# Kernel tuning notes

Hardware: AMD Instinct MI355X
Metric: run time of the kernel (lower is better)

## Reference

```python
import jax, jax.numpy as jnp
import numpy as np

N_MFS = 2
N_FEATURES = 12
OUTPUT_DIM = 8
BATCH = 4096
N_RULES = N_MFS ** N_FEATURES  # 4096


def _rule_indices(n_features, n_mfs):
    r = np.arange(n_mfs ** n_features)
    # mixed-radix digits: indices[rule, feat] = (rule // n_mfs**feat) % n_mfs
    return np.stack([(r // (n_mfs ** f)) % n_mfs for f in range(n_features)], axis=1).astype(np.int32)


def setup_inputs() -> dict:
    key = jax.random.key(0)
    ks = jax.random.split(key, 6)
    x = jax.random.normal(ks[0], (BATCH, N_FEATURES), dtype=jnp.float32)
    center_base = jax.random.uniform(ks[1], (N_FEATURES, 1), minval=-1.0, maxval=0.0, dtype=jnp.float32)
    center_delta_raw = jax.random.normal(ks[2], (N_FEATURES, N_MFS - 1), dtype=jnp.float32) * 0.5
    width_raw = jax.random.normal(ks[3], (N_FEATURES, N_MFS), dtype=jnp.float32) * 0.5
    fan = N_RULES * N_FEATURES + OUTPUT_DIM
    limit = float(np.sqrt(6.0 / fan))
    consequent_p = jax.random.uniform(ks[4], (N_RULES, N_FEATURES, OUTPUT_DIM), minval=-limit, maxval=limit, dtype=jnp.float32)
    consequent_r = jnp.zeros((N_RULES, OUTPUT_DIM), dtype=jnp.float32)
    rule_mf_indices = jnp.asarray(_rule_indices(N_FEATURES, N_MFS))
    return {"x": x, "center_base": center_base, "center_delta_raw": center_delta_raw,
            "width_raw": width_raw, "consequent_p": consequent_p, "consequent_r": consequent_r,
            "rule_mf_indices": rule_mf_indices}


def reference(x, center_base, center_delta_raw, width_raw, consequent_p, consequent_r, rule_mf_indices):
    # ordered centers: base + cumsum(softplus(delta) + 1e-3)
    gaps = jax.nn.softplus(center_delta_raw) + 1e-3          # (F, M-1)
    offsets = jnp.cumsum(gaps, axis=1)
    centers = jnp.concatenate([center_base, center_base + offsets], axis=1)  # (F, M)
    widths = jax.nn.softplus(width_raw) + 1e-3                # (F, M)

    # Gaussian memberships: (B, F, M)
    d = x[:, :, None] - centers[None, :, :]
    memberships = jnp.exp(-jnp.square(d) / (2.0 * jnp.square(widths)[None, :, :]))

    # rule firing: product over features of gathered memberships (loop over small fixed F)
    firing = jnp.ones((x.shape[0], rule_mf_indices.shape[0]), dtype=x.dtype)  # (B, R)
    for f in range(memberships.shape[1]):
        firing = firing * memberships[:, f, :][:, rule_mf_indices[:, f]]
    firing_norm = firing / (jnp.sum(firing, axis=1, keepdims=True) + 1e-8)

    # per-rule linear consequents: (B, R, O)
    rule_outputs = jnp.einsum('bf,rfo->bro', x, consequent_p) + consequent_r[None, :, :]
    # weighted reduce over rules: (B, O)
    output = jnp.einsum('br,bro->bo', firing_norm, rule_outputs)
    return output
```

## Files before the change

### kernel.cpp

```cpp
#include <hip/hip_runtime.h>
#include <math.h>

#define NF 12
#define NB 4096
#define NR 4096
#define NO 8

typedef float f32x4v __attribute__((ext_vector_type(4)));
typedef short bf16x8 __attribute__((ext_vector_type(8)));
typedef unsigned int uint32x4 __attribute__((ext_vector_type(4)));

#define PT2_BYTES (128 * 8 * 512 * 2)
#define PARAMS_OFF PT2_BYTES
#define WS_NEED (PT2_BYTES + 2048)
#define PT_ELEMS (112 * 4096)

__device__ __forceinline__ float softplus_f(float v) {
    return fmaxf(v, 0.0f) + log1pf(__expf(-fabsf(v)));
}
__device__ __forceinline__ unsigned short f2bf(float f) {
    unsigned u = __float_as_uint(f);
    u += 0x7FFFu + ((u >> 16) & 1u);
    return (unsigned short)(u >> 16);
}
__device__ __forceinline__ unsigned cvt_pk_bf16(float a, float b) {
    unsigned r;
    asm("v_cvt_pk_bf16_f32 %0, %1, %2" : "=v"(r) : "v"(a), "v"(b));
    return r;
}

__device__ __forceinline__ void build_split(f32x4v va, f32x4v vb,
                                            bf16x8& ah, bf16x8& al) {
    unsigned h0 = cvt_pk_bf16(va[0], va[1]), h1 = cvt_pk_bf16(va[2], va[3]);
    unsigned h2 = cvt_pk_bf16(vb[0], vb[1]), h3 = cvt_pk_bf16(vb[2], vb[3]);
    f32x4v hia = { __uint_as_float(h0 << 16), __uint_as_float(h0 & 0xFFFF0000u),
                   __uint_as_float(h1 << 16), __uint_as_float(h1 & 0xFFFF0000u) };
    f32x4v hib = { __uint_as_float(h2 << 16), __uint_as_float(h2 & 0xFFFF0000u),
                   __uint_as_float(h3 << 16), __uint_as_float(h3 & 0xFFFF0000u) };
    f32x4v ea = va - hia;
    f32x4v eb = vb - hib;
    unsigned q0 = cvt_pk_bf16(ea[0], ea[1]), q1 = cvt_pk_bf16(ea[2], ea[3]);
    unsigned q2 = cvt_pk_bf16(eb[0], eb[1]), q3 = cvt_pk_bf16(eb[2], eb[3]);
    union { uint32x4 u; bf16x8 v; } A, B;
    A.u = (uint32x4){h0, h1, h2, h3};
    B.u = (uint32x4){q0, q1, q2, q3};
    ah = A.v; al = B.v;
}

__global__ __launch_bounds__(512) void anfis_prep2(
    const float* __restrict__ cp, const float* __restrict__ cr,
    const float* __restrict__ center_base, const float* __restrict__ cdr,
    const float* __restrict__ wr,
    unsigned short* __restrict__ PT2, float* __restrict__ params,
    float* __restrict__ out_zero)
{
    __shared__ float s_cp[32 * 97];
    __shared__ float s_cr[32 * 8];
    const int kt = blockIdx.x;
    const int tid = threadIdx.x;

    if (kt < 64) out_zero[(size_t)kt * 512 + tid] = 0.0f;

    {
        const float4* cp4 = (const float4*)(cp + (size_t)kt * 32 * 96);
        for (int i = tid; i < 768; i += 512) {
            float4 v = cp4[i];
            int r = i / 24, c4 = i - r * 24;
            float* d = &s_cp[r * 97 + c4 * 4];
            d[0] = v.x; d[1] = v.y; d[2] = v.z; d[3] = v.w;
        }
        if (tid < 64) {
            float4 v = ((const float4*)(cr + (size_t)kt * 32 * 8))[tid];
            float* d = &s_cr[tid * 4];
            d[0] = v.x; d[1] = v.y; d[2] = v.z; d[3] = v.w;
        }
    }
    __syncthreads();

    const int g = tid >> 7, col = (tid >> 3) & 15, e = tid & 7;
    const int rr = g * 8 + e;
    #pragma unroll
    for (int j = 0; j < 8; ++j) {
        int n = j * 16 + col;
        float v = 0.f;
        if (n < 96) v = s_cp[rr * 97 + n];
        else if (n < 104) v = s_cr[rr * 8 + (n - 96)];
        PT2[(size_t)(kt * 8 + j) * 512 + tid] = f2bf(v);
    }

    if (kt == 0 && tid < NF) {
        float c0 = center_base[tid];
        float gap = softplus_f(cdr[tid]) + 1e-3f;
        float w0 = softplus_f(wr[tid * 2 + 0]) + 1e-3f;
        float w1 = softplus_f(wr[tid * 2 + 1]) + 1e-3f;
        params[tid * 4 + 0] = c0;
        params[tid * 4 + 1] = c0 + gap;
        params[tid * 4 + 2] = -0.5f / (w0 * w0);
        params[tid * 4 + 3] = -0.5f / (w1 * w1);
    }
}

__global__ __launch_bounds__(512, 4) void anfis_main7(
    const float* __restrict__ x,
    const unsigned short* __restrict__ PT2,
    const float* __restrict__ params,
    float* __restrict__ out)
{
    __shared__ float s_params[48];
    __shared__ float s_mf[64 * 24];
    __shared__ float s_prod[64 * 8];
    __shared__ float s_rcp[64];
    __shared__ float s_x[64 * 12];
    __shared__ float s_low[64 * 36];
    __shared__ float s_highT[16 * 64];
    __shared__ __align__(16) unsigned char s_B[2 * 16384];

    const int tid = threadIdx.x;
    const int bid = blockIdx.x;
    const int ks = bid & 7;
    const int mt = bid >> 3;
    const int b0 = mt * 64;
    const int kt0 = ks * 16;

    const int w = tid >> 6, l = tid & 63;

    const unsigned char* ptBase = (const unsigned char*)PT2;
    #define STAGE(c, buf) do {                                                        \
        if (w != 7) {                                                                 \
            const unsigned char* gb = ptBase + ((size_t)(kt0 + 2 * (c)) << 13);       \
            unsigned char* lb = &s_B[(buf) * 16384];                                  \
            __builtin_amdgcn_global_load_lds(                                         \
                (const __attribute__((address_space(1))) void*)(gb + w * 1024 + l * 16),  \
                (__attribute__((address_space(3))) void*)(lb + w * 1024), 16, 0, 0);  \
            __builtin_amdgcn_global_load_lds(                                         \
                (const __attribute__((address_space(1))) void*)(gb + (8 + w) * 1024 + l * 16), \
                (__attribute__((address_space(3))) void*)(lb + (8 + w) * 1024), 16, 0, 0);\
        }                                                                             \
    } while (0)

    STAGE(0, 0);
    STAGE(1, 1);

    if (tid < 192) {
        float4 v = ((const float4*)(x + (size_t)b0 * NF))[tid];
        float* d = &s_x[tid * 4];
        d[0] = v.x; d[1] = v.y; d[2] = v.z; d[3] = v.w;
    }
    if (tid >= 500) {
        int f = tid - 500;
        ((float4*)s_params)[f] = ((const float4*)params)[f];
    }
    __syncthreads();

    if (tid < 384) {
        int row = tid / 6, fp = tid - row * 6;
        float pr = 1.f;
        #pragma unroll
        for (int h = 0; h < 2; ++h) {
            int f = fp + h * 6;
            float xv = s_x[row * 12 + f];
            float4 pm = *(const float4*)&s_params[f * 4];
            float d0 = xv - pm.x, d1 = xv - pm.y;
            float m0 = __expf(d0 * d0 * pm.z);
            float m1 = __expf(d1 * d1 * pm.w);
            s_mf[row * 24 + f * 2 + 0] = m0;
            s_mf[row * 24 + f * 2 + 1] = m1;
            pr *= (m0 + m1);
        }
        s_prod[row * 8 + fp] = pr;
    }
    __syncthreads();
    if (tid < 64) {
        float S = 1.f;
        #pragma unroll
        for (int i = 0; i < 6; ++i) S *= s_prod[tid * 8 + i];
        s_rcp[tid] = 1.0f / (S + 1e-8f);
    }
    __syncthreads();

    {
        int row = tid >> 3, w8 = tid & 7;
        const float* mr = &s_mf[row * 24];
        #pragma unroll
        for (int i = 0; i < 4; ++i) {
            int ee = w8 * 4 + i;
            float p = 1.f;
            #pragma unroll
            for (int f = 0; f < 5; ++f) p *= mr[f * 2 + ((ee >> f) & 1)];
            s_low[row * 36 + ee] = p;
        }
        float rc = s_rcp[row];
        #pragma unroll
        for (int i = 0; i < 2; ++i) {
            int t = w8 * 2 + i;
            int ktg = kt0 + t;
            float p = rc;
            #pragma unroll
            for (int ff = 0; ff < 7; ++ff) p *= mr[(5 + ff) * 2 + ((ktg >> ff) & 1)];
            s_highT[t * 64 + row] = p;
        }
    }
    __syncthreads();

    const int rp = w >> 2, cq = w & 3;
    const int col = l & 15, g = l >> 4;
    const int nj = (cq < 3) ? 2 : 1;
    const int jb = cq * 2;

    bf16x8 ah[2], al[2];
    #pragma unroll
    for (int i = 0; i < 2; ++i) {
        int rowA = (rp * 2 + i) * 16 + col;
        f32x4v lo0 = *(const f32x4v*)&s_low[rowA * 36 + g * 8];
        f32x4v lo1 = *(const f32x4v*)&s_low[rowA * 36 + g * 8 + 4];
        build_split(lo0, lo1, ah[i], al[i]);
    }

    f32x4v acc[2][2];
    #pragma unroll
    for (int i = 0; i < 2; ++i)
        #pragma unroll
        for (int jj = 0; jj < 2; ++jj) acc[i][jj] = (f32x4v){0.f, 0.f, 0.f, 0.f};
    const f32x4v z4 = (f32x4v){0.f, 0.f, 0.f, 0.f};

    const int hoff0 = (rp * 2 + 0) * 16 + g * 4;
    const int hoff1 = (rp * 2 + 1) * 16 + g * 4;

    #pragma unroll 1
    for (int c = 0; c < 8; ++c) {
        const int cur = c & 1;
        if (c >= 1 && c + 1 < 8) STAGE(c + 1, cur ^ 1);
        #pragma unroll
        for (int kt2 = 0; kt2 < 2; ++kt2) {
            const int t = c * 2 + kt2;
            const unsigned char* base = &s_B[cur * 16384 + kt2 * 8192 + l * 16];
            bf16x8 fr0 = *(const bf16x8*)(base + jb * 1024);
            f32x4v hv0 = *(const f32x4v*)&s_highT[t * 64 + hoff0];
            f32x4v hv1 = *(const f32x4v*)&s_highT[t * 64 + hoff1];
            f32x4v q00, q10;
            q00 = __builtin_amdgcn_mfma_f32_16x16x32_bf16(ah[0], fr0, z4, 0, 0, 0);
            q00 = __builtin_amdgcn_mfma_f32_16x16x32_bf16(al[0], fr0, q00, 0, 0, 0);
            q10 = __builtin_amdgcn_mfma_f32_16x16x32_bf16(ah[1], fr0, z4, 0, 0, 0);
            q10 = __builtin_amdgcn_mfma_f32_16x16x32_bf16(al[1], fr0, q10, 0, 0, 0);
            acc[0][0] += hv0 * q00;
            acc[1][0] += hv1 * q10;
            if (nj == 2) {
                bf16x8 fr1 = *(const bf16x8*)(base + (jb + 1) * 1024);
                f32x4v q01, q11;
                q01 = __builtin_amdgcn_mfma_f32_16x16x32_bf16(ah[0], fr1, z4, 0, 0, 0);
                q01 = __builtin_amdgcn_mfma_f32_16x16x32_bf16(al[0], fr1, q01, 0, 0, 0);
                q11 = __builtin_amdgcn_mfma_f32_16x16x32_bf16(ah[1], fr1, z4, 0, 0, 0);
                q11 = __builtin_amdgcn_mfma_f32_16x16x32_bf16(al[1], fr1, q11, 0, 0, 0);
                acc[0][1] += hv0 * q01;
                acc[1][1] += hv1 * q11;
            }
        }
        __syncthreads();
    }
    #undef STAGE

    float* s_acc = (float*)s_B;
    #pragma unroll
    for (int i = 0; i < 2; ++i) {
        #pragma unroll
        for (int jj = 0; jj < 2; ++jj) {
            if (jj < nj) {
                int j = jb + jj;
                #pragma unroll
                for (int q = 0; q < 4; ++q)
                    s_acc[((rp * 2 + i) * 16 + g * 4 + q) * 116 + j * 16 + col] = acc[i][jj][q];
            }
        }
    }
    __syncthreads();
    {
        const int row = tid >> 3, o = tid & 7;
        const float* ar = &s_acc[row * 116];
        float t = ar[96 + o];
        #pragma unroll
        for (int f = 0; f < NF; ++f) t = fmaf(s_x[row * 12 + f], ar[f * 8 + o], t);
        atomicAdd(&out[(size_t)(b0 + row) * NO + o], t);
    }
}

__global__ __launch_bounds__(256) void anfis_prep(
    const float* __restrict__ cp, const float* __restrict__ cr,
    unsigned short* __restrict__ PT)
{
    const int n = blockIdx.x;
    const int t = threadIdx.x;
    if (n < 96) {
        #pragma unroll
        for (int i = 0; i < 16; ++i) { int r = i * 256 + t; PT[n * 4096 + r] = f2bf(cp[r * 96 + n]); }
    } else if (n < 104) {
        const int o = n - 96;
        #pragma unroll
        for (int i = 0; i < 16; ++i) { int r = i * 256 + t; PT[n * 4096 + r] = f2bf(cr[r * 8 + o]); }
    } else {
        #pragma unroll
        for (int i = 0; i < 16; ++i) PT[n * 4096 + i * 256 + t] = 0;
    }
}

__global__ __launch_bounds__(512) void anfis_mfma(
    const float* __restrict__ x,
    const float* __restrict__ center_base,
    const float* __restrict__ center_delta_raw,
    const float* __restrict__ width_raw,
    const unsigned short* __restrict__ PT,
    float* __restrict__ out)
{
    __shared__ float s_mem[16 * 26];
    __shared__ float s_low[16 * 36];
    __shared__ float s_high[16 * 132];
    __shared__ float s_red[8 * 16 * 113];

    const int tid = threadIdx.x;
    const int b0 = blockIdx.x * 16;

    if (tid < 16) {
        const int b = b0 + tid;
        float S = 1.0f;
        #pragma unroll
        for (int f = 0; f < NF; ++f) {
            float cb  = center_base[f];
            float gap = softplus_f(center_delta_raw[f]) + 1e-3f;
            float c0 = cb, c1 = cb + gap;
            float w0 = softplus_f(width_raw[f * 2 + 0]) + 1e-3f;
            float w1 = softplus_f(width_raw[f * 2 + 1]) + 1e-3f;
            float xv = x[b * NF + f];
            float d0 = xv - c0, d1 = xv - c1;
            float m0 = __expf(-d0 * d0 / (2.0f * w0 * w0));
            float m1 = __expf(-d1 * d1 / (2.0f * w1 * w1));
            s_mem[tid * 26 + f * 2 + 0] = m0;
            s_mem[tid * 26 + f * 2 + 1] = m1;
            S *= (m0 + m1);
        }
        s_mem[tid * 26 + 24] = 1.0f / (S + 1e-8f);
    }
    __syncthreads();
    if (tid < 256) {
        const int row = tid >> 4, w16 = tid & 15;
        const float* mrow = &s_mem[row * 26];
        #pragma unroll
        for (int e = 2 * w16; e <= 2 * w16 + 1; ++e) {
            float p = 1.0f;
            #pragma unroll
            for (int f = 0; f < 5; ++f) p *= mrow[f * 2 + ((e >> f) & 1)];
            s_low[row * 36 + e] = p;
        }
        float rcp = mrow[24];
        #pragma unroll
        for (int i = 0; i < 8; ++i) {
            int e = w16 + 16 * i;
            float p = rcp;
            #pragma unroll
            for (int ff = 0; ff < 7; ++ff) p *= mrow[(5 + ff) * 2 + ((e >> ff) & 1)];
            s_high[row * 132 + e] = p;
        }
    }
    __syncthreads();

    const int w = tid >> 6;
    const int l = tid & 63;
    const int col = l & 15;
    const int g   = l >> 4;

    f32x4v lo0 = *(const f32x4v*)&s_low[col * 36 + g * 8];
    f32x4v lo1 = *(const f32x4v*)&s_low[col * 36 + g * 8 + 4];
    f32x4v hq0 = *(const f32x4v*)&s_high[col * 132 + w * 16 + 0];
    f32x4v hq1 = *(const f32x4v*)&s_high[col * 132 + w * 16 + 4];
    f32x4v hq2 = *(const f32x4v*)&s_high[col * 132 + w * 16 + 8];
    f32x4v hq3 = *(const f32x4v*)&s_high[col * 132 + w * 16 + 12];

    const unsigned short* pB = PT + (size_t)col * 4096 + g * 8 + w * 512;

    f32x4v acc[7];
    #pragma unroll
    for (int j = 0; j < 7; ++j) acc[j] = (f32x4v){0.f, 0.f, 0.f, 0.f};

    bf16x8 bf[2][7];
    #pragma unroll
    for (int j = 0; j < 7; ++j) bf[0][j] = *(const bf16x8*)(pB + j * 65536 + 0 * 32);
    #pragma unroll
    for (int j = 0; j < 7; ++j) bf[1][j] = *(const bf16x8*)(pB + j * 65536 + 1 * 32);

    #pragma unroll
    for (int s = 0; s < 16; ++s) {
        const float hv = (s < 4) ? hq0[s & 3] : (s < 8) ? hq1[s & 3]
                        : (s < 12) ? hq2[s & 3] : hq3[s & 3];
        bf16x8 ah, al;
        #pragma unroll
        for (int e = 0; e < 8; ++e) {
            float v = ((e < 4) ? lo0[e & 3] : lo1[e & 3]) * hv;
            unsigned short h = f2bf(v);
            float vh = __uint_as_float(((unsigned)h) << 16);
            ah[e] = (short)h;
            al[e] = (short)f2bf(v - vh);
        }
        #pragma unroll
        for (int j = 0; j < 7; ++j) {
            acc[j] = __builtin_amdgcn_mfma_f32_16x16x32_bf16(ah, bf[s & 1][j], acc[j], 0, 0, 0);
            acc[j] = __builtin_amdgcn_mfma_f32_16x16x32_bf16(al, bf[s & 1][j], acc[j], 0, 0, 0);
        }
        if (s + 2 < 16) {
            #pragma unroll
            for (int j = 0; j < 7; ++j)
                bf[s & 1][j] = *(const bf16x8*)(pB + j * 65536 + (s + 2) * 32);
        }
    }

    #pragma unroll
    for (int j = 0; j < 7; ++j)
        #pragma unroll
        for (int q = 0; q < 4; ++q)
            s_red[(w * 16 + g * 4 + q) * 113 + j * 16 + col] = acc[j][q];
    __syncthreads();

    if (tid < 128) {
        const int row = tid >> 3, o = tid & 7;
        float xr[NF];
        #pragma unroll
        for (int f = 0; f < NF; ++f) xr[f] = x[(b0 + row) * NF + f];
        float outv = 0.0f;
        #pragma unroll
        for (int ww = 0; ww < 8; ++ww) {
            const float* ar = &s_red[(ww * 16 + row) * 113];
            float t2 = ar[96 + o];
            #pragma unroll
            for (int f = 0; f < NF; ++f) t2 = fmaf(xr[f], ar[f * 8 + o], t2);
            outv += t2;
        }
        out[(b0 + row) * NO + o] = outv;
    }
}

extern "C" void kernel_launch(void* const* d_in, const int* in_sizes, int n_in,
                              void* d_out, int out_size, void* d_ws, size_t ws_size,
                              hipStream_t stream) {
    const float* x   = (const float*)d_in[0];
    const float* cb  = (const float*)d_in[1];
    const float* cdr = (const float*)d_in[2];
    const float* wr  = (const float*)d_in[3];
    const float* cp  = (const float*)d_in[4];
    const float* cr  = (const float*)d_in[5];
    float* out = (float*)d_out;

    if (ws_size >= (size_t)WS_NEED) {
        unsigned short* PT2 = (unsigned short*)d_ws;
        float* params = (float*)((char*)d_ws + PARAMS_OFF);
        anfis_prep2<<<128, 512, 0, stream>>>(cp, cr, cb, cdr, wr, PT2, params, out);
        anfis_main7<<<512, 512, 0, stream>>>(x, PT2, params, out);
    } else if (ws_size >= (size_t)PT_ELEMS * sizeof(unsigned short)) {
        unsigned short* PT = (unsigned short*)d_ws;
        anfis_prep<<<112, 256, 0, stream>>>(cp, cr, PT);
        anfis_mfma<<<NB / 16, 512, 0, stream>>>(x, cb, cdr, wr, PT, out);
    }
}
```

Baseline: 21.27 us.

## Triple-buffer B tiles with explicit vmcnt waits and compute params in-kernel

The rule-table staging loop moves from a double buffer with a full __syncthreads per chunk to a three-slot ring buffer. Each chunk is prefetched two iterations ahead, and consumption is gated by explicit s_waitcnt vmcnt plus a bare s_barrier. The main kernel also computes the softplus membership parameters itself instead of reading them from the prep kernel's workspace. The intent is to overlap global-to-LDS loads with MFMA work and cut sync stalls. In exchange LDS use grows by 16KB per block, which may lower occupancy, and the hand-written vmcnt counting is fragile.

```diff
diff --git a/kernel.cpp b/kernel.cpp
--- a/kernel.cpp
+++ b/kernel.cpp
@@ -100,10 +100,11 @@
     }
 }
 
-__global__ __launch_bounds__(512, 4) void anfis_main7(
+__global__ __launch_bounds__(512, 4) void anfis_main8(
     const float* __restrict__ x,
+    const float* __restrict__ center_base, const float* __restrict__ cdr,
+    const float* __restrict__ wr,
     const unsigned short* __restrict__ PT2,
-    const float* __restrict__ params,
     float* __restrict__ out)
 {
     __shared__ float s_params[48];
@@ -113,7 +114,7 @@
     __shared__ float s_x[64 * 12];
     __shared__ float s_low[64 * 36];
     __shared__ float s_highT[16 * 64];
-    __shared__ __align__(16) unsigned char s_B[2 * 16384];
+    __shared__ __align__(16) unsigned char s_B[3 * 16384];
 
     const int tid = threadIdx.x;
     const int bid = blockIdx.x;
@@ -146,9 +147,16 @@
         float* d = &s_x[tid * 4];
         d[0] = v.x; d[1] = v.y; d[2] = v.z; d[3] = v.w;
     }
-    if (tid >= 500) {
+    if (tid >= 500 && tid < 500 + NF) {
         int f = tid - 500;
-        ((float4*)s_params)[f] = ((const float4*)params)[f];
+        float c0 = center_base[f];
+        float gap = softplus_f(cdr[f]) + 1e-3f;
+        float w0 = softplus_f(wr[f * 2 + 0]) + 1e-3f;
+        float w1 = softplus_f(wr[f * 2 + 1]) + 1e-3f;
+        s_params[f * 4 + 0] = c0;
+        s_params[f * 4 + 1] = c0 + gap;
+        s_params[f * 4 + 2] = -0.5f / (w0 * w0);
+        s_params[f * 4 + 3] = -0.5f / (w1 * w1);
     }
     __syncthreads();
 
@@ -226,14 +234,20 @@
     const int hoff0 = (rp * 2 + 0) * 16 + g * 4;
     const int hoff1 = (rp * 2 + 1) * 16 + g * 4;
 
+    int bc = 0;
     #pragma unroll 1
     for (int c = 0; c < 8; ++c) {
-        const int cur = c & 1;
-        if (c >= 1 && c + 1 < 8) STAGE(c + 1, cur ^ 1);
+        if (c < 7) asm volatile("s_waitcnt vmcnt(2)" ::: "memory");
+        else       asm volatile("s_waitcnt vmcnt(0)" ::: "memory");
+        __builtin_amdgcn_s_barrier();
+        if (c + 2 < 8) {
+            int st = (bc >= 1) ? bc - 1 : 2;
+            STAGE(c + 2, st);
+        }
         #pragma unroll
         for (int kt2 = 0; kt2 < 2; ++kt2) {
             const int t = c * 2 + kt2;
-            const unsigned char* base = &s_B[cur * 16384 + kt2 * 8192 + l * 16];
+            const unsigned char* base = &s_B[bc * 16384 + kt2 * 8192 + l * 16];
             bf16x8 fr0 = *(const bf16x8*)(base + jb * 1024);
             f32x4v hv0 = *(const f32x4v*)&s_highT[t * 64 + hoff0];
             f32x4v hv1 = *(const f32x4v*)&s_highT[t * 64 + hoff1];
@@ -255,9 +269,10 @@
                 acc[1][1] += hv1 * q11;
             }
         }
-        __syncthreads();
+        bc = (bc == 2) ? 0 : bc + 1;
     }
     #undef STAGE
+    __syncthreads();
 
     float* s_acc = (float*)s_B;
     #pragma unroll
@@ -450,7 +465,7 @@
         unsigned short* PT2 = (unsigned short*)d_ws;
         float* params = (float*)((char*)d_ws + PARAMS_OFF);
         anfis_prep2<<<128, 512, 0, stream>>>(cp, cr, cb, cdr, wr, PT2, params, out);
-        anfis_main7<<<512, 512, 0, stream>>>(x, PT2, params, out);
+        anfis_main8<<<512, 512, 0, stream>>>(x, cb, cdr, wr, PT2, out);
     } else if (ws_size >= (size_t)PT_ELEMS * sizeof(unsigned short)) {
         unsigned short* PT = (unsigned short*)d_ws;
         anfis_prep<<<112, 256, 0, stream>>>(cp, cr, PT);
```

After: 21.99 us. +3.4%, slower.

## Replace atomic split-K accumulation with partial buffer and reduction kernel

Applied to the files above, without the earlier changes.

The main kernel now writes per-K-split partial outputs to a workspace buffer instead of atomically adding into the output, and a new small kernel sums the 8 partials. Membership parameters are computed inside the main kernel rather than in the prep kernel. Memberships are kept in registers per thread, which removes two shared-memory passes and barriers. This avoids atomic contention and the need to zero the output, at the cost of an extra kernel launch and extra global traffic for the partials.

```diff
diff --git a/kernel.cpp b/kernel.cpp
--- a/kernel.cpp
+++ b/kernel.cpp
@@ -11,8 +11,9 @@
 typedef unsigned int uint32x4 __attribute__((ext_vector_type(4)));
 
 #define PT2_BYTES (128 * 8 * 512 * 2)
-#define PARAMS_OFF PT2_BYTES
-#define WS_NEED (PT2_BYTES + 2048)
+#define PPART_OFF PT2_BYTES
+#define PPART_BYTES (8 * NB * NO * 4)
+#define WS_NEED (PT2_BYTES + PPART_BYTES)
 #define PT_ELEMS (112 * 4096)
 
 __device__ __forceinline__ float softplus_f(float v) {
@@ -47,19 +48,14 @@
     ah = A.v; al = B.v;
 }
 
-__global__ __launch_bounds__(512) void anfis_prep2(
+__global__ __launch_bounds__(512) void anfis_prep3(
     const float* __restrict__ cp, const float* __restrict__ cr,
-    const float* __restrict__ center_base, const float* __restrict__ cdr,
-    const float* __restrict__ wr,
-    unsigned short* __restrict__ PT2, float* __restrict__ params,
-    float* __restrict__ out_zero)
+    unsigned short* __restrict__ PT2)
 {
     __shared__ float s_cp[32 * 97];
     __shared__ float s_cr[32 * 8];
     const int kt = blockIdx.x;
     const int tid = threadIdx.x;
-
-    if (kt < 64) out_zero[(size_t)kt * 512 + tid] = 0.0f;
 
     {
         const float4* cp4 = (const float4*)(cp + (size_t)kt * 32 * 96);
@@ -87,29 +83,16 @@
         else if (n < 104) v = s_cr[rr * 8 + (n - 96)];
         PT2[(size_t)(kt * 8 + j) * 512 + tid] = f2bf(v);
     }
-
-    if (kt == 0 && tid < NF) {
-        float c0 = center_base[tid];
-        float gap = softplus_f(cdr[tid]) + 1e-3f;
-        float w0 = softplus_f(wr[tid * 2 + 0]) + 1e-3f;
-        float w1 = softplus_f(wr[tid * 2 + 1]) + 1e-3f;
-        params[tid * 4 + 0] = c0;
-        params[tid * 4 + 1] = c0 + gap;
-        params[tid * 4 + 2] = -0.5f / (w0 * w0);
-        params[tid * 4 + 3] = -0.5f / (w1 * w1);
-    }
-}
-
-__global__ __launch_bounds__(512, 4) void anfis_main7(
+}
+
+__global__ __launch_bounds__(512, 4) void anfis_main9(
     const float* __restrict__ x,
+    const float* __restrict__ center_base, const float* __restrict__ cdr,
+    const float* __restrict__ wr,
     const unsigned short* __restrict__ PT2,
-    const float* __restrict__ params,
-    float* __restrict__ out)
+    float* __restrict__ Ppart)
 {
     __shared__ float s_params[48];
-    __shared__ float s_mf[64 * 24];
-    __shared__ float s_prod[64 * 8];
-    __shared__ float s_rcp[64];
     __shared__ float s_x[64 * 12];
     __shared__ float s_low[64 * 36];
     __shared__ float s_highT[16 * 64];
@@ -146,57 +129,52 @@
         float* d = &s_x[tid * 4];
         d[0] = v.x; d[1] = v.y; d[2] = v.z; d[3] = v.w;
     }
-    if (tid >= 500) {
+    if (tid >= 500 && tid < 500 + NF) {
         int f = tid - 500;
-        ((float4*)s_params)[f] = ((const float4*)params)[f];
-    }
-    __syncthreads();
-
-    if (tid < 384) {
-        int row = tid / 6, fp = tid - row * 6;
-        float pr = 1.f;
-        #pragma unroll
-        for (int h = 0; h < 2; ++h) {
-            int f = fp + h * 6;
-            float xv = s_x[row * 12 + f];
+        float c0 = center_base[f];
+        float gap = softplus_f(cdr[f]) + 1e-3f;
+        float w0 = softplus_f(wr[f * 2 + 0]) + 1e-3f;
+        float w1 = softplus_f(wr[f * 2 + 1]) + 1e-3f;
+        s_params[f * 4 + 0] = c0;
+        s_params[f * 4 + 1] = c0 + gap;
+        s_params[f * 4 + 2] = -0.5f / (w0 * w0);
+        s_params[f * 4 + 3] = -0.5f / (w1 * w1);
+    }
+    __syncthreads();
+
+    {
+        const int row = tid >> 3, w8 = tid & 7;
+        const float* xr = &s_x[row * 12];
+        float m0a[NF], m1a[NF];
+        float S = 1.f;
+        #pragma unroll
+        for (int f = 0; f < NF; ++f) {
             float4 pm = *(const float4*)&s_params[f * 4];
+            float xv = xr[f];
             float d0 = xv - pm.x, d1 = xv - pm.y;
-            float m0 = __expf(d0 * d0 * pm.z);
-            float m1 = __expf(d1 * d1 * pm.w);
-            s_mf[row * 24 + f * 2 + 0] = m0;
-            s_mf[row * 24 + f * 2 + 1] = m1;
-            pr *= (m0 + m1);
-        }
-        s_prod[row * 8 + fp] = pr;
-    }
-    __syncthreads();
-    if (tid < 64) {
-        float S = 1.f;
-        #pragma unroll
-        for (int i = 0; i < 6; ++i) S *= s_prod[tid * 8 + i];
-        s_rcp[tid] = 1.0f / (S + 1e-8f);
-    }
-    __syncthreads();
-
-    {
-        int row = tid >> 3, w8 = tid & 7;
-        const float* mr = &s_mf[row * 24];
+            float e0 = __expf(d0 * d0 * pm.z);
+            float e1 = __expf(d1 * d1 * pm.w);
+            m0a[f] = e0; m1a[f] = e1;
+            S *= (e0 + e1);
+        }
+        float rc = 1.0f / (S + 1e-8f);
         #pragma unroll
         for (int i = 0; i < 4; ++i) {
             int ee = w8 * 4 + i;
             float p = 1.f;
             #pragma unroll
-            for (int f = 0; f < 5; ++f) p *= mr[f * 2 + ((ee >> f) & 1)];
+            for (int f = 0; f < 5; ++f)
+                p *= ((ee >> f) & 1) ? m1a[f] : m0a[f];
             s_low[row * 36 + ee] = p;
         }
-        float rc = s_rcp[row];
         #pragma unroll
         for (int i = 0; i < 2; ++i) {
             int t = w8 * 2 + i;
             int ktg = kt0 + t;
             float p = rc;
             #pragma unroll
-            for (int ff = 0; ff < 7; ++ff) p *= mr[(5 + ff) * 2 + ((ktg >> ff) & 1)];
+            for (int ff = 0; ff < 7; ++ff)
+                p *= ((ktg >> ff) & 1) ? m1a[5 + ff] : m0a[5 + ff];
             s_highT[t * 64 + row] = p;
         }
     }
@@ -279,8 +257,22 @@
         float t = ar[96 + o];
         #pragma unroll
         for (int f = 0; f < NF; ++f) t = fmaf(s_x[row * 12 + f], ar[f * 8 + o], t);
-        atomicAdd(&out[(size_t)(b0 + row) * NO + o], t);
-    }
+        Ppart[((size_t)ks * NB + b0 + row) * NO + o] = t;
+    }
+}
+
+__global__ __launch_bounds__(256) void anfis_red2(
+    const float* __restrict__ Ppart, float* __restrict__ out)
+{
+    const int i = blockIdx.x * 256 + threadIdx.x;
+    const float4* p = (const float4*)Ppart;
+    float4 a = p[i];
+    #pragma unroll
+    for (int ksi = 1; ksi < 8; ++ksi) {
+        float4 b = p[(size_t)ksi * (NB * NO / 4) + i];
+        a.x += b.x; a.y += b.y; a.z += b.z; a.w += b.w;
+    }
+    ((float4*)out)[i] = a;
 }
 
 __global__ __launch_bounds__(256) void anfis_prep(
@@ -448,9 +440,10 @@
 
     if (ws_size >= (size_t)WS_NEED) {
         unsigned short* PT2 = (unsigned short*)d_ws;
-        float* params = (float*)((char*)d_ws + PARAMS_OFF);
-        anfis_prep2<<<128, 512, 0, stream>>>(cp, cr, cb, cdr, wr, PT2, params, out);
-        anfis_main7<<<512, 512, 0, stream>>>(x, PT2, params, out);
+        float* Ppart = (float*)((char*)d_ws + PPART_OFF);
+        anfis_prep3<<<128, 512, 0, stream>>>(cp, cr, PT2);
+        anfis_main9<<<512, 512, 0, stream>>>(x, cb, cdr, wr, PT2, Ppart);
+        anfis_red2<<<NB * NO / 4 / 256, 256, 0, stream>>>(Ppart, out);
     } else if (ws_size >= (size_t)PT_ELEMS * sizeof(unsigned short)) {
         unsigned short* PT = (unsigned short*)d_ws;
         anfis_prep<<<112, 256, 0, stream>>>(cp, cr, PT);
```

Measured after the change: 24.49 us. +15.2%, slower.

## Split K across wave halves so each wave covers all 64 rows

Applied to the files above, without the earlier changes.

Each wave previously covered two 16-row A tiles and looped over both k-subtiles per chunk. Now each wave holds all four row tiles and handles only one k-subtile, chosen by wave half. The two halves are then combined through shared memory with an extra barrier-separated accumulate pass. The aim is better reuse of each B fragment across more MFMAs and fewer B fragment reads per MFMA. The cost is more registers for the A fragments and accumulators, plus an added reduction step at the end.

```diff
diff --git a/kernel.cpp b/kernel.cpp
--- a/kernel.cpp
+++ b/kernel.cpp
@@ -100,7 +100,7 @@
     }
 }
 
-__global__ __launch_bounds__(512, 4) void anfis_main7(
+__global__ __launch_bounds__(512, 4) void anfis_main11(
     const float* __restrict__ x,
     const unsigned short* __restrict__ PT2,
     const float* __restrict__ params,
@@ -202,57 +202,56 @@
     }
     __syncthreads();
 
-    const int rp = w >> 2, cq = w & 3;
+    const int h = w >> 2, cq = w & 3;
     const int col = l & 15, g = l >> 4;
     const int nj = (cq < 3) ? 2 : 1;
     const int jb = cq * 2;
 
-    bf16x8 ah[2], al[2];
-    #pragma unroll
-    for (int i = 0; i < 2; ++i) {
-        int rowA = (rp * 2 + i) * 16 + col;
+    bf16x8 ah[4], al[4];
+    #pragma unroll
+    for (int i = 0; i < 4; ++i) {
+        int rowA = i * 16 + col;
         f32x4v lo0 = *(const f32x4v*)&s_low[rowA * 36 + g * 8];
         f32x4v lo1 = *(const f32x4v*)&s_low[rowA * 36 + g * 8 + 4];
         build_split(lo0, lo1, ah[i], al[i]);
     }
 
-    f32x4v acc[2][2];
-    #pragma unroll
-    for (int i = 0; i < 2; ++i)
+    f32x4v acc[4][2];
+    #pragma unroll
+    for (int i = 0; i < 4; ++i)
         #pragma unroll
         for (int jj = 0; jj < 2; ++jj) acc[i][jj] = (f32x4v){0.f, 0.f, 0.f, 0.f};
     const f32x4v z4 = (f32x4v){0.f, 0.f, 0.f, 0.f};
-
-    const int hoff0 = (rp * 2 + 0) * 16 + g * 4;
-    const int hoff1 = (rp * 2 + 1) * 16 + g * 4;
 
     #pragma unroll 1
     for (int c = 0; c < 8; ++c) {
         const int cur = c & 1;
         if (c >= 1 && c + 1 < 8) STAGE(c + 1, cur ^ 1);
-        #pragma unroll
-        for (int kt2 = 0; kt2 < 2; ++kt2) {
-            const int t = c * 2 + kt2;
-            const unsigned char* base = &s_B[cur * 16384 + kt2 * 8192 + l * 16];
-            bf16x8 fr0 = *(const bf16x8*)(base + jb * 1024);
-            f32x4v hv0 = *(const f32x4v*)&s_highT[t * 64 + hoff0];
-            f32x4v hv1 = *(const f32x4v*)&s_highT[t * 64 + hoff1];
-            f32x4v q00, q10;
-            q00 = __builtin_amdgcn_mfma_f32_16x16x32_bf16(ah[0], fr0, z4, 0, 0, 0);
-            q00 = __builtin_amdgcn_mfma_f32_16x16x32_bf16(al[0], fr0, q00, 0, 0, 0);
-            q10 = __builtin_amdgcn_mfma_f32_16x16x32_bf16(ah[1], fr0, z4, 0, 0, 0);
-            q10 = __builtin_amdgcn_mfma_f32_16x16x32_bf16(al[1], fr0, q10, 0, 0, 0);
-            acc[0][0] += hv0 * q00;
-            acc[1][0] += hv1 * q10;
-            if (nj == 2) {
-                bf16x8 fr1 = *(const bf16x8*)(base + (jb + 1) * 1024);
-                f32x4v q01, q11;
-                q01 = __builtin_amdgcn_mfma_f32_16x16x32_bf16(ah[0], fr1, z4, 0, 0, 0);
-                q01 = __builtin_amdgcn_mfma_f32_16x16x32_bf16(al[0], fr1, q01, 0, 0, 0);
-                q11 = __builtin_amdgcn_mfma_f32_16x16x32_bf16(ah[1], fr1, z4, 0, 0, 0);
-                q11 = __builtin_amdgcn_mfma_f32_16x16x32_bf16(al[1], fr1, q11, 0, 0, 0);
-                acc[0][1] += hv0 * q01;
-                acc[1][1] += hv1 * q11;
+        {
+            const int t = c * 2 + h;
+            const unsigned char* base = &s_B[cur * 16384 + h * 8192 + l * 16];
+            f32x4v hv0 = *(const f32x4v*)&s_highT[t * 64 +  0 + g * 4];
+            f32x4v hv1 = *(const f32x4v*)&s_highT[t * 64 + 16 + g * 4];
+            f32x4v hv2 = *(const f32x4v*)&s_highT[t * 64 + 32 + g * 4];
+            f32x4v hv3 = *(const f32x4v*)&s_highT[t * 64 + 48 + g * 4];
+            #pragma unroll
+            for (int jj = 0; jj < 2; ++jj) {
+                if (jj < nj) {
+                    bf16x8 fr = *(const bf16x8*)(base + (jb + jj) * 1024);
+                    f32x4v q0, q1, q2, q3;
+                    q0 = __builtin_amdgcn_mfma_f32_16x16x32_bf16(ah[0], fr, z4, 0, 0, 0);
+                    q1 = __builtin_amdgcn_mfma_f32_16x16x32_bf16(ah[1], fr, z4, 0, 0, 0);
+                    q2 = __builtin_amdgcn_mfma_f32_16x16x32_bf16(ah[2], fr, z4, 0, 0, 0);
+                    q3 = __builtin_amdgcn_mfma_f32_16x16x32_bf16(ah[3], fr, z4, 0, 0, 0);
+                    q0 = __builtin_amdgcn_mfma_f32_16x16x32_bf16(al[0], fr, q0, 0, 0, 0);
+                    q1 = __builtin_amdgcn_mfma_f32_16x16x32_bf16(al[1], fr, q1, 0, 0, 0);
+                    q2 = __builtin_amdgcn_mfma_f32_16x16x32_bf16(al[2], fr, q2, 0, 0, 0);
+                    q3 = __builtin_amdgcn_mfma_f32_16x16x32_bf16(al[3], fr, q3, 0, 0, 0);
+                    acc[0][jj] += hv0 * q0;
+                    acc[1][jj] += hv1 * q1;
+                    acc[2][jj] += hv2 * q2;
+                    acc[3][jj] += hv3 * q3;
+                }
             }
         }
         __syncthreads();
@@ -260,17 +259,30 @@
     #undef STAGE
 
     float* s_acc = (float*)s_B;
-    #pragma unroll
-    for (int i = 0; i < 2; ++i) {
-        #pragma unroll
-        for (int jj = 0; jj < 2; ++jj) {
-            if (jj < nj) {
-                int j = jb + jj;
-                #pragma unroll
-                for (int q = 0; q < 4; ++q)
-                    s_acc[((rp * 2 + i) * 16 + g * 4 + q) * 116 + j * 16 + col] = acc[i][jj][q];
-            }
-        }
+    if (h == 0) {
+        #pragma unroll
+        for (int i = 0; i < 4; ++i)
+            #pragma unroll
+            for (int jj = 0; jj < 2; ++jj)
+                if (jj < nj) {
+                    int j = jb + jj;
+                    #pragma unroll
+                    for (int q = 0; q < 4; ++q)
+                        s_acc[(i * 16 + g * 4 + q) * 116 + j * 16 + col] = acc[i][jj][q];
+                }
+    }
+    __syncthreads();
+    if (h == 1) {
+        #pragma unroll
+        for (int i = 0; i < 4; ++i)
+            #pragma unroll
+            for (int jj = 0; jj < 2; ++jj)
+                if (jj < nj) {
+                    int j = jb + jj;
+                    #pragma unroll
+                    for (int q = 0; q < 4; ++q)
+                        s_acc[(i * 16 + g * 4 + q) * 116 + j * 16 + col] += acc[i][jj][q];
+                }
     }
     __syncthreads();
     {
@@ -450,7 +462,7 @@
         unsigned short* PT2 = (unsigned short*)d_ws;
         float* params = (float*)((char*)d_ws + PARAMS_OFF);
         anfis_prep2<<<128, 512, 0, stream>>>(cp, cr, cb, cdr, wr, PT2, params, out);
-        anfis_main7<<<512, 512, 0, stream>>>(x, PT2, params, out);
+        anfis_main11<<<512, 512, 0, stream>>>(x, PT2, params, out);
     } else if (ws_size >= (size_t)PT_ELEMS * sizeof(unsigned short)) {
         unsigned short* PT = (unsigned short*)d_ws;
         anfis_prep<<<112, 256, 0, stream>>>(cp, cr, PT);
```

Result: slower. 22.18 us (+4.3%).
